# Kernel optimization log

Hardware: AMD Instinct MI355X
Metric: run time of the kernel (lower is better)

Reference implementation:

```python
import jax, jax.numpy as jnp
import numpy as np


def setup_inputs() -> dict:
    key = jax.random.key(0)
    kq, kk, kv = jax.random.split(key, 3)
    B, L, Q, H, E = 8, 128, 8, 8, 64
    S, P = 128, 8
    queries = jax.random.normal(kq, (B, L, Q, H, E), dtype=jnp.float32)
    keys = jax.random.normal(kk, (B, S, P, H, E), dtype=jnp.float32)
    values = jax.random.normal(kv, (B, S, P, H, E), dtype=jnp.float32)
    attn_mask = jnp.zeros((1,), dtype=bool)  # unused by the module
    return {"queries": queries, "keys": keys, "values": values, "attn_mask": attn_mask}


def reference(queries, keys, values, attn_mask):
    # queries: [B,L,Q,H,E]; keys/values: [B,S,P,H,E]
    B, L, Q, H, E = queries.shape
    S, P = values.shape[1], values.shape[2]
    scale = 1.0 / np.sqrt(E).astype(np.float32)
    # scores: [B,S,P,L,Q,H]
    scores = jnp.einsum('blqhe,bsphe->bsplqh', queries, keys)
    # softmax over joint (S,P) axis
    scaled = (scale * scores).reshape(B, S * P, L, Q, H)
    attn = jax.nn.softmax(scaled, axis=1).reshape(B, S, P, L, Q, H)
    # dropout is identity in eval / with p=0.0
    V = jnp.einsum('bsphe,bsplqh->blqhe', values, attn)
    return V
```

## Files before the change

### kernel.cpp

```cpp
#include <hip/hip_runtime.h>
#include <hip/hip_bf16.h>

typedef __attribute__((ext_vector_type(4))) float f32x4;
typedef __attribute__((ext_vector_type(16))) float f32x16;
typedef __attribute__((ext_vector_type(8))) short bf16x8;
typedef __attribute__((ext_vector_type(4))) unsigned u32x4;

#define MFMA32(a, b, c) __builtin_amdgcn_mfma_f32_32x32x16_bf16(a, b, c, 0, 0, 0)
#define EXP2(x) __builtin_amdgcn_exp2f(x)

constexpr int NQ = 1024;
constexpr int NK = 1024;
constexpr int RS = 512;
constexpr int Ec = 64;
constexpr int KT = 128;
constexpr int NT = NK / KT;
constexpr float QSCALE2 = 0.125f * 1.4426950408889634f;

__device__ __forceinline__ short f2bf(float x) {
    return (short)__builtin_bit_cast(unsigned short, __float2bfloat16(x));
}

__device__ __forceinline__ bf16x8 pack2(float4 a, float4 b) {
    bf16x8 r;
    r[0] = f2bf(a.x); r[1] = f2bf(a.y); r[2] = f2bf(a.z); r[3] = f2bf(a.w);
    r[4] = f2bf(b.x); r[5] = f2bf(b.y); r[6] = f2bf(b.z); r[7] = f2bf(b.w);
    return r;
}

__device__ __forceinline__ bf16x8 pack2s(float4 a, float4 b, float s) {
    bf16x8 r;
    r[0] = f2bf(a.x * s); r[1] = f2bf(a.y * s); r[2] = f2bf(a.z * s); r[3] = f2bf(a.w * s);
    r[4] = f2bf(b.x * s); r[5] = f2bf(b.y * s); r[6] = f2bf(b.z * s); r[7] = f2bf(b.w * s);
    return r;
}

__device__ __forceinline__ unsigned cvtpk(float a, float b) {
    unsigned lo = (unsigned short)__builtin_bit_cast(unsigned short, __float2bfloat16(a));
    unsigned hi = (unsigned short)__builtin_bit_cast(unsigned short, __float2bfloat16(b));
    return lo | (hi << 16);
}

__device__ __forceinline__ void gload16(const short* src, short* dst) {
    __builtin_amdgcn_global_load_lds((const __attribute__((address_space(1))) void*)src,
                                     (__attribute__((address_space(3))) void*)dst, 16, 0, 0);
}

__global__ __launch_bounds__(256, 4)
void cvt_kv(const float* __restrict__ Kg, const float* __restrict__ Vg,
            short* __restrict__ Kbf, short* __restrict__ Vt) {
    __shared__ __attribute__((aligned(16))) short Vl[64][72];
    const int tid  = threadIdx.x;
    const int head = blockIdx.x >> 4;
    const int kb   = blockIdx.x & 15;
    const int b    = head >> 3, h = head & 7;
    const int row  = tid >> 2, q = tid & 3;

    const size_t gin = (((size_t)(b * NK + kb * 64 + row)) * 8 + h) * 64 + q * 16;
    const float4* kp = (const float4*)(Kg + gin);
    float4 k0 = kp[0], k1 = kp[1], k2 = kp[2], k3 = kp[3];
    short* kout = Kbf + ((size_t)head * NK + kb * 64 + row) * 64 + q * 16;
    ((bf16x8*)kout)[0] = pack2(k0, k1);
    ((bf16x8*)kout)[1] = pack2(k2, k3);

    const float4* vp = (const float4*)(Vg + gin);
    float4 v0 = vp[0], v1 = vp[1], v2 = vp[2], v3 = vp[3];
    const float vv[16] = {v0.x, v0.y, v0.z, v0.w, v1.x, v1.y, v1.z, v1.w,
                          v2.x, v2.y, v2.z, v2.w, v3.x, v3.y, v3.z, v3.w};
#pragma unroll
    for (int j = 0; j < 16; ++j) Vl[q * 16 + j][row] = f2bf(vv[j]);
    __syncthreads();
    short* vout = Vt + ((size_t)head * Ec + row) * NK + kb * 64 + q * 16;
    ((bf16x8*)vout)[0] = *(const bf16x8*)&Vl[row][q * 16];
    ((bf16x8*)vout)[1] = *(const bf16x8*)&Vl[row][q * 16 + 8];
}

__global__ __launch_bounds__(256, 2)
void fully_attn_kernel(const float* __restrict__ Qg, const short* __restrict__ Kbf,
                       const short* __restrict__ Vt, float* __restrict__ Og) {
    __shared__ __attribute__((aligned(16))) short Kl[2][KT][64];
    __shared__ __attribute__((aligned(16))) short Vl[2][64][KT];

    const int tid  = threadIdx.x;
    const int lane = tid & 63;
    const int wv   = tid >> 6;
    const int ql   = lane & 31;
    const int hi   = lane >> 5;
    const int swz  = (lane & 7) << 4;

    const int bid  = blockIdx.x;
    const int head = (bid & 7) * 8 + (bid >> 6);
    const int qb   = (bid >> 3) & 7;
    const int b    = head >> 3, h = head & 7;

    const size_t headQ = (size_t)b * NQ * RS + (size_t)h * Ec;
    const short* KbfH = Kbf + (size_t)head * NK * Ec;
    const short* VtH  = Vt + (size_t)head * Ec * NK;

    const int qrow = qb * 128 + wv * 32 + ql;
    const float* qp = Qg + headQ + (size_t)qrow * RS;
    bf16x8 qf[4];
#pragma unroll
    for (int j = 0; j < 4; ++j) {
        const float4* q4 = (const float4*)(qp + j * 16 + hi * 8);
        qf[j] = pack2s(q4[0], q4[1], QSCALE2);
    }

    const int klocal = lane >> 3;
    const int kj     = (lane & 7) ^ (klocal & 7);
    const int vlocal = lane >> 4;

#define STAGE(buf, tt)                                                            \
    {                                                                             \
        _Pragma("unroll")                                                         \
        for (int s = 0; s < 4; ++s)                                               \
            gload16(KbfH + (size_t)((tt) * KT + wv * 32 + s * 8 + klocal) * 64 +  \
                        kj * 8,                                                   \
                    &Kl[buf][wv * 32 + s * 8][0]);                                \
        _Pragma("unroll")                                                         \
        for (int s = 0; s < 4; ++s)                                               \
            gload16(VtH + (size_t)(wv * 16 + s * 4 + vlocal) * NK + (tt) * KT +   \
                        (((lane & 15) ^ ((s * 4 + vlocal) & 7)) * 8),             \
                    &Vl[buf][wv * 16 + s * 4][0]);                                \
    }

    STAGE(0, 0);
    __syncthreads();

    float l_r = 0.0f;
    f32x16 o0 = (f32x16)(0.0f), o1 = (f32x16)(0.0f);

    int cur = 0;
    for (int t = 0; t < NT; ++t) {
        if (t + 1 < NT) STAGE(cur ^ 1, t + 1);

        bf16x8 kf[4][4];
#pragma unroll
        for (int kt = 0; kt < 4; ++kt) {
            const char* kr = (const char*)&Kl[cur][kt * 32 + ql][0];
#pragma unroll
            for (int j = 0; j < 4; ++j)
                kf[kt][j] = *(const bf16x8*)(kr + ((j * 32 + hi * 16) ^ swz));
        }
        f32x16 p[4];
        __builtin_amdgcn_s_setprio(1);
#pragma unroll
        for (int kt = 0; kt < 4; ++kt) {
            f32x16 acc = (f32x16)(0.0f);
#pragma unroll
            for (int j = 0; j < 4; ++j) acc = MFMA32(kf[kt][j], qf[j], acc);
            p[kt] = acc;
        }
        __builtin_amdgcn_s_setprio(0);

        bf16x8 vf0[8], vf1[8];
#pragma unroll
        for (int m = 0; m < 8; ++m) {
            const int cb = (m * 32 + hi * 16) ^ swz;
            vf0[m] = *(const bf16x8*)((const char*)&Vl[cur][ql][0] + cb);
            vf1[m] = *(const bf16x8*)((const char*)&Vl[cur][32 + ql][0] + cb);
        }

        float rs0 = 0.f, rs1 = 0.f, rs2 = 0.f, rs3 = 0.f;
#pragma unroll
        for (int kt = 0; kt < 4; ++kt)
#pragma unroll
            for (int i = 0; i < 16; i += 4) {
                float e0 = EXP2(p[kt][i + 0]);
                float e1 = EXP2(p[kt][i + 1]);
                float e2 = EXP2(p[kt][i + 2]);
                float e3 = EXP2(p[kt][i + 3]);
                p[kt][i + 0] = e0; p[kt][i + 1] = e1;
                p[kt][i + 2] = e2; p[kt][i + 3] = e3;
                rs0 += e0; rs1 += e1; rs2 += e2; rs3 += e3;
            }
        l_r += (rs0 + rs1) + (rs2 + rs3);

        __builtin_amdgcn_s_setprio(1);
#pragma unroll
        for (int m = 0; m < 8; ++m) {
            const int kt = m >> 1, r0 = (m & 1) * 8;
            unsigned a0 = cvtpk(p[kt][r0 + 0], p[kt][r0 + 1]);
            unsigned a1 = cvtpk(p[kt][r0 + 2], p[kt][r0 + 3]);
            unsigned b0 = cvtpk(p[kt][r0 + 4], p[kt][r0 + 5]);
            unsigned b1 = cvtpk(p[kt][r0 + 6], p[kt][r0 + 7]);
            asm("v_permlane32_swap_b32 %0, %1" : "+v"(a0), "+v"(b0));
            asm("v_permlane32_swap_b32 %0, %1" : "+v"(a1), "+v"(b1));
            u32x4 w = {a0, a1, b0, b1};
            bf16x8 pf = __builtin_bit_cast(bf16x8, w);
            o0 = MFMA32(vf0[m], pf, o0);
            o1 = MFMA32(vf1[m], pf, o1);
        }
        __builtin_amdgcn_s_setprio(0);

        __syncthreads();
        cur ^= 1;
    }

    l_r += __shfl_xor(l_r, 32);
    const float inv = 1.0f / l_r;
    float* op = Og + headQ + (size_t)qrow * RS;
#pragma unroll
    for (int bnk = 0; bnk < 4; ++bnk) {
        float4 s0 = {o0[bnk * 4 + 0] * inv, o0[bnk * 4 + 1] * inv,
                     o0[bnk * 4 + 2] * inv, o0[bnk * 4 + 3] * inv};
        float4 s1 = {o1[bnk * 4 + 0] * inv, o1[bnk * 4 + 1] * inv,
                     o1[bnk * 4 + 2] * inv, o1[bnk * 4 + 3] * inv};
        *(float4*)(op + bnk * 8 + hi * 4)      = s0;
        *(float4*)(op + 32 + bnk * 8 + hi * 4) = s1;
    }
}

extern "C" void kernel_launch(void* const* d_in, const int* in_sizes, int n_in,
                              void* d_out, int out_size, void* d_ws, size_t ws_size,
                              hipStream_t stream) {
    const float* Qg = (const float*)d_in[0];
    const float* Kg = (const float*)d_in[1];
    const float* Vg = (const float*)d_in[2];
    float* Og = (float*)d_out;

    short* Kbf = (short*)d_ws;
    short* Vt  = (short*)d_ws + (size_t)64 * NK * Ec;

    hipLaunchKernelGGL(cvt_kv, dim3(64 * 16), dim3(256), 0, stream, Kg, Vg, Kbf, Vt);
    hipLaunchKernelGGL(fully_attn_kernel, dim3(512), dim3(256), 0, stream,
                       Qg, Kbf, Vt, Og);
}
```

Before: 43.85 us.

## Split K tile into halves to interleave QK^T MFMA with softmax and PV

```diff
diff --git a/kernel.cpp b/kernel.cpp
--- a/kernel.cpp
+++ b/kernel.cpp
@@ -124,79 +124,87 @@
                     &Vl[buf][wv * 16 + s * 4][0]);                                \
     }
 
+#define QKT_HALF(s0, s1, kbase)                                                   \
+    {                                                                             \
+        const char* kr0 = (const char*)&Kl[cur][(kbase) + ql][0];                 \
+        const char* kr1 = (const char*)&Kl[cur][(kbase) + 32 + ql][0];            \
+        bf16x8 kf0[4], kf1[4];                                                    \
+        _Pragma("unroll")                                                         \
+        for (int j = 0; j < 4; ++j) {                                             \
+            kf0[j] = *(const bf16x8*)(kr0 + ((j * 32 + hi * 16) ^ swz));          \
+            kf1[j] = *(const bf16x8*)(kr1 + ((j * 32 + hi * 16) ^ swz));          \
+        }                                                                         \
+        __builtin_amdgcn_s_setprio(1);                                            \
+        s0 = MFMA32(kf0[0], qf[0], (f32x16)(0.0f));                               \
+        s1 = MFMA32(kf1[0], qf[0], (f32x16)(0.0f));                               \
+        s0 = MFMA32(kf0[1], qf[1], s0);                                           \
+        s1 = MFMA32(kf1[1], qf[1], s1);                                           \
+        s0 = MFMA32(kf0[2], qf[2], s0);                                           \
+        s1 = MFMA32(kf1[2], qf[2], s1);                                           \
+        s0 = MFMA32(kf0[3], qf[3], s0);                                           \
+        s1 = MFMA32(kf1[3], qf[3], s1);                                           \
+        __builtin_amdgcn_s_setprio(0);                                            \
+    }
+
+#define FINISH_HALF(s0, s1, mbase)                                                \
+    {                                                                             \
+        float rs0 = 0.f, rs1 = 0.f, rs2 = 0.f, rs3 = 0.f;                         \
+        _Pragma("unroll")                                                         \
+        for (int i = 0; i < 16; i += 4) {                                         \
+            s0[i + 0] = EXP2(s0[i + 0]); s0[i + 1] = EXP2(s0[i + 1]);             \
+            s0[i + 2] = EXP2(s0[i + 2]); s0[i + 3] = EXP2(s0[i + 3]);             \
+            s1[i + 0] = EXP2(s1[i + 0]); s1[i + 1] = EXP2(s1[i + 1]);             \
+            s1[i + 2] = EXP2(s1[i + 2]); s1[i + 3] = EXP2(s1[i + 3]);             \
+            rs0 += s0[i + 0] + s1[i + 0]; rs1 += s0[i + 1] + s1[i + 1];           \
+            rs2 += s0[i + 2] + s1[i + 2]; rs3 += s0[i + 3] + s1[i + 3];           \
+        }                                                                         \
+        l_r += (rs0 + rs1) + (rs2 + rs3);                                         \
+        const char* vr0 = (const char*)&Vl[cur][ql][0];                           \
+        const char* vr1 = (const char*)&Vl[cur][32 + ql][0];                      \
+        __builtin_amdgcn_s_setprio(1);                                            \
+        _Pragma("unroll")                                                         \
+        for (int m = 0; m < 4; ++m) {                                             \
+            f32x16& sk = (m < 2) ? s0 : s1;                                       \
+            const int r0 = (m & 1) * 8;                                           \
+            unsigned a0 = cvtpk(sk[r0 + 0], sk[r0 + 1]);                          \
+            unsigned a1 = cvtpk(sk[r0 + 2], sk[r0 + 3]);                          \
+            unsigned b0 = cvtpk(sk[r0 + 4], sk[r0 + 5]);                          \
+            unsigned b1 = cvtpk(sk[r0 + 6], sk[r0 + 7]);                          \
+            asm("v_permlane32_swap_b32 %0, %1" : "+v"(a0), "+v"(b0));             \
+            asm("v_permlane32_swap_b32 %0, %1" : "+v"(a1), "+v"(b1));             \
+            u32x4 w = {a0, a1, b0, b1};                                           \
+            bf16x8 pf = __builtin_bit_cast(bf16x8, w);                            \
+            const int cb = (((mbase) + m) * 32 + hi * 16) ^ swz;                  \
+            bf16x8 v0 = *(const bf16x8*)(vr0 + cb);                               \
+            bf16x8 v1 = *(const bf16x8*)(vr1 + cb);                               \
+            if (m & 1) { o0b = MFMA32(v0, pf, o0b); o1b = MFMA32(v1, pf, o1b); }  \
+            else       { o0a = MFMA32(v0, pf, o0a); o1a = MFMA32(v1, pf, o1a); }  \
+        }                                                                         \
+        __builtin_amdgcn_s_setprio(0);                                            \
+    }
+
     STAGE(0, 0);
     __syncthreads();
 
     float l_r = 0.0f;
-    f32x16 o0 = (f32x16)(0.0f), o1 = (f32x16)(0.0f);
+    f32x16 o0a = (f32x16)(0.0f), o0b = (f32x16)(0.0f);
+    f32x16 o1a = (f32x16)(0.0f), o1b = (f32x16)(0.0f);
 
     int cur = 0;
     for (int t = 0; t < NT; ++t) {
+        f32x16 sA0, sA1, sB0, sB1;
+        QKT_HALF(sA0, sA1, 0);
         if (t + 1 < NT) STAGE(cur ^ 1, t + 1);
-
-        bf16x8 kf[4][4];
-#pragma unroll
-        for (int kt = 0; kt < 4; ++kt) {
-            const char* kr = (const char*)&Kl[cur][kt * 32 + ql][0];
-#pragma unroll
-            for (int j = 0; j < 4; ++j)
-                kf[kt][j] = *(const bf16x8*)(kr + ((j * 32 + hi * 16) ^ swz));
-        }
-        f32x16 p[4];
-        __builtin_amdgcn_s_setprio(1);
-#pragma unroll
-        for (int kt = 0; kt < 4; ++kt) {
-            f32x16 acc = (f32x16)(0.0f);
-#pragma unroll
-            for (int j = 0; j < 4; ++j) acc = MFMA32(kf[kt][j], qf[j], acc);
-            p[kt] = acc;
-        }
-        __builtin_amdgcn_s_setprio(0);
-
-        bf16x8 vf0[8], vf1[8];
-#pragma unroll
-        for (int m = 0; m < 8; ++m) {
-            const int cb = (m * 32 + hi * 16) ^ swz;
-            vf0[m] = *(const bf16x8*)((const char*)&Vl[cur][ql][0] + cb);
-            vf1[m] = *(const bf16x8*)((const char*)&Vl[cur][32 + ql][0] + cb);
-        }
-
-        float rs0 = 0.f, rs1 = 0.f, rs2 = 0.f, rs3 = 0.f;
-#pragma unroll
-        for (int kt = 0; kt < 4; ++kt)
-#pragma unroll
-            for (int i = 0; i < 16; i += 4) {
-                float e0 = EXP2(p[kt][i + 0]);
-                float e1 = EXP2(p[kt][i + 1]);
-                float e2 = EXP2(p[kt][i + 2]);
-                float e3 = EXP2(p[kt][i + 3]);
-                p[kt][i + 0] = e0; p[kt][i + 1] = e1;
-                p[kt][i + 2] = e2; p[kt][i + 3] = e3;
-                rs0 += e0; rs1 += e1; rs2 += e2; rs3 += e3;
-            }
-        l_r += (rs0 + rs1) + (rs2 + rs3);
-
-        __builtin_amdgcn_s_setprio(1);
-#pragma unroll
-        for (int m = 0; m < 8; ++m) {
-            const int kt = m >> 1, r0 = (m & 1) * 8;
-            unsigned a0 = cvtpk(p[kt][r0 + 0], p[kt][r0 + 1]);
-            unsigned a1 = cvtpk(p[kt][r0 + 2], p[kt][r0 + 3]);
-            unsigned b0 = cvtpk(p[kt][r0 + 4], p[kt][r0 + 5]);
-            unsigned b1 = cvtpk(p[kt][r0 + 6], p[kt][r0 + 7]);
-            asm("v_permlane32_swap_b32 %0, %1" : "+v"(a0), "+v"(b0));
-            asm("v_permlane32_swap_b32 %0, %1" : "+v"(a1), "+v"(b1));
-            u32x4 w = {a0, a1, b0, b1};
-            bf16x8 pf = __builtin_bit_cast(bf16x8, w);
-            o0 = MFMA32(vf0[m], pf, o0);
-            o1 = MFMA32(vf1[m], pf, o1);
-        }
-        __builtin_amdgcn_s_setprio(0);
-
+        QKT_HALF(sB0, sB1, 64);
+        FINISH_HALF(sA0, sA1, 0);
+        FINISH_HALF(sB0, sB1, 4);
         __syncthreads();
         cur ^= 1;
     }
 
+    f32x16 o0, o1;
+#pragma unroll
+    for (int i = 0; i < 16; ++i) { o0[i] = o0a[i] + o0b[i]; o1[i] = o1a[i] + o1b[i]; }
     l_r += __shfl_xor(l_r, 32);
     const float inv = 1.0f / l_r;
     float* op = Og + headQ + (size_t)qrow * RS;
```

Result: faster. 42.71 us (-2.6%).

## Load K and V fragments directly from global memory instead of LDS staging

Applied to the files above, without the earlier changes.

```diff
diff --git a/kernel.cpp b/kernel.cpp
--- a/kernel.cpp
+++ b/kernel.cpp
@@ -41,11 +41,6 @@
     return lo | (hi << 16);
 }
 
-__device__ __forceinline__ void gload16(const short* src, short* dst) {
-    __builtin_amdgcn_global_load_lds((const __attribute__((address_space(1))) void*)src,
-                                     (__attribute__((address_space(3))) void*)dst, 16, 0, 0);
-}
-
 __global__ __launch_bounds__(256, 4)
 void cvt_kv(const float* __restrict__ Kg, const float* __restrict__ Vg,
             short* __restrict__ Kbf, short* __restrict__ Vt) {
@@ -78,15 +73,11 @@
 __global__ __launch_bounds__(256, 2)
 void fully_attn_kernel(const float* __restrict__ Qg, const short* __restrict__ Kbf,
                        const short* __restrict__ Vt, float* __restrict__ Og) {
-    __shared__ __attribute__((aligned(16))) short Kl[2][KT][64];
-    __shared__ __attribute__((aligned(16))) short Vl[2][64][KT];
-
     const int tid  = threadIdx.x;
     const int lane = tid & 63;
     const int wv   = tid >> 6;
     const int ql   = lane & 31;
     const int hi   = lane >> 5;
-    const int swz  = (lane & 7) << 4;
 
     const int bid  = blockIdx.x;
     const int head = (bid & 7) * 8 + (bid >> 6);
@@ -94,8 +85,8 @@
     const int b    = head >> 3, h = head & 7;
 
     const size_t headQ = (size_t)b * NQ * RS + (size_t)h * Ec;
-    const short* KbfH = Kbf + (size_t)head * NK * Ec;
-    const short* VtH  = Vt + (size_t)head * Ec * NK;
+    const short* Kh = Kbf + (size_t)head * NK * Ec;
+    const short* Vh = Vt + (size_t)head * Ec * NK;
 
     const int qrow = qb * 128 + wv * 32 + ql;
     const float* qp = Qg + headQ + (size_t)qrow * RS;
@@ -106,59 +97,37 @@
         qf[j] = pack2s(q4[0], q4[1], QSCALE2);
     }
 
-    const int klocal = lane >> 3;
-    const int kj     = (lane & 7) ^ (klocal & 7);
-    const int vlocal = lane >> 4;
-
-#define STAGE(buf, tt)                                                            \
-    {                                                                             \
-        _Pragma("unroll")                                                         \
-        for (int s = 0; s < 4; ++s)                                               \
-            gload16(KbfH + (size_t)((tt) * KT + wv * 32 + s * 8 + klocal) * 64 +  \
-                        kj * 8,                                                   \
-                    &Kl[buf][wv * 32 + s * 8][0]);                                \
-        _Pragma("unroll")                                                         \
-        for (int s = 0; s < 4; ++s)                                               \
-            gload16(VtH + (size_t)(wv * 16 + s * 4 + vlocal) * NK + (tt) * KT +   \
-                        (((lane & 15) ^ ((s * 4 + vlocal) & 7)) * 8),             \
-                    &Vl[buf][wv * 16 + s * 4][0]);                                \
-    }
-
-    STAGE(0, 0);
-    __syncthreads();
+    const short* Vrow0 = Vh + (size_t)ql * NK + hi * 8;
+    const short* Vrow1 = Vh + (size_t)(32 + ql) * NK + hi * 8;
 
     float l_r = 0.0f;
     f32x16 o0 = (f32x16)(0.0f), o1 = (f32x16)(0.0f);
 
-    int cur = 0;
     for (int t = 0; t < NT; ++t) {
-        if (t + 1 < NT) STAGE(cur ^ 1, t + 1);
+        const int kb = t * KT;
 
-        bf16x8 kf[4][4];
+        f32x16 p[4];
 #pragma unroll
         for (int kt = 0; kt < 4; ++kt) {
-            const char* kr = (const char*)&Kl[cur][kt * 32 + ql][0];
-#pragma unroll
-            for (int j = 0; j < 4; ++j)
-                kf[kt][j] = *(const bf16x8*)(kr + ((j * 32 + hi * 16) ^ swz));
-        }
-        f32x16 p[4];
-        __builtin_amdgcn_s_setprio(1);
-#pragma unroll
-        for (int kt = 0; kt < 4; ++kt) {
-            f32x16 acc = (f32x16)(0.0f);
-#pragma unroll
-            for (int j = 0; j < 4; ++j) acc = MFMA32(kf[kt][j], qf[j], acc);
+            const short* kr = Kh + (size_t)(kb + kt * 32 + ql) * 64 + hi * 8;
+            bf16x8 k0 = *(const bf16x8*)(kr + 0);
+            bf16x8 k1 = *(const bf16x8*)(kr + 16);
+            bf16x8 k2 = *(const bf16x8*)(kr + 32);
+            bf16x8 k3 = *(const bf16x8*)(kr + 48);
+            __builtin_amdgcn_s_setprio(1);
+            f32x16 acc = MFMA32(k0, qf[0], (f32x16)(0.0f));
+            acc = MFMA32(k1, qf[1], acc);
+            acc = MFMA32(k2, qf[2], acc);
+            acc = MFMA32(k3, qf[3], acc);
+            __builtin_amdgcn_s_setprio(0);
             p[kt] = acc;
         }
-        __builtin_amdgcn_s_setprio(0);
 
         bf16x8 vf0[8], vf1[8];
 #pragma unroll
         for (int m = 0; m < 8; ++m) {
-            const int cb = (m * 32 + hi * 16) ^ swz;
-            vf0[m] = *(const bf16x8*)((const char*)&Vl[cur][ql][0] + cb);
-            vf1[m] = *(const bf16x8*)((const char*)&Vl[cur][32 + ql][0] + cb);
+            vf0[m] = *(const bf16x8*)(Vrow0 + kb + m * 16);
+            vf1[m] = *(const bf16x8*)(Vrow1 + kb + m * 16);
         }
 
         float rs0 = 0.f, rs1 = 0.f, rs2 = 0.f, rs3 = 0.f;
@@ -192,9 +161,6 @@
             o1 = MFMA32(vf1[m], pf, o1);
         }
         __builtin_amdgcn_s_setprio(0);
-
-        __syncthreads();
-        cur ^= 1;
     }
 
     l_r += __shfl_xor(l_r, 32);
```

Result: slower. 79.44 us (+81.1%).
